# Kernel optimization log

Hardware: AMD Instinct MI355X
Metric: run time of the kernel (lower is better)

## Reference

```python
import jax, jax.numpy as jnp
import numpy as np

D = 2048
N_HEADS = 16
N_KV = 4
HEAD_DIM = D // N_HEADS  # 128
N_REP = N_HEADS // N_KV  # 4
B, S = 2, 2048


def setup_inputs() -> dict:
    key = jax.random.key(0)
    ks = jax.random.split(key, 5)
    scale = 0.02
    return {
        "x": jax.random.normal(ks[0], (B, S, D), dtype=jnp.float32),
        "wq": jax.random.normal(ks[1], (D, N_HEADS * HEAD_DIM), dtype=jnp.float32) * scale,
        "wk": jax.random.normal(ks[2], (D, N_KV * HEAD_DIM), dtype=jnp.float32) * scale,
        "wv": jax.random.normal(ks[3], (D, N_KV * HEAD_DIM), dtype=jnp.float32) * scale,
        "wo": jax.random.normal(ks[4], (N_HEADS * HEAD_DIM, D), dtype=jnp.float32) * scale,
    }


def reference(x, wq, wk, wv, wo):
    b, s, _ = x.shape
    # projections
    xq = (x @ wq).reshape(b, s, N_HEADS, HEAD_DIM)
    xk = (x @ wk).reshape(b, s, N_KV, HEAD_DIM)
    xv = (x @ wv).reshape(b, s, N_KV, HEAD_DIM)
    # GQA: group queries per kv head -> [b, n_kv, n_rep, s, d]
    xq = xq.transpose(0, 2, 1, 3).reshape(b, N_KV, N_REP, s, HEAD_DIM)
    xk = xk.transpose(0, 2, 1, 3)  # [b, n_kv, s, d]
    xv = xv.transpose(0, 2, 1, 3)
    scale = 1.0 / jnp.sqrt(jnp.asarray(HEAD_DIM, dtype=x.dtype))
    scores = jnp.einsum('bkrqd,bkvd->bkrqv', xq, xk) * scale  # [b,n_kv,n_rep,s,s]
    causal = jnp.triu(jnp.ones((s, s), dtype=bool), k=1)
    scores = jnp.where(causal, jnp.asarray(-jnp.inf, dtype=scores.dtype), scores)
    probs = jax.nn.softmax(scores, axis=-1)
    out = jnp.einsum('bkrqv,bkvd->bkrqd', probs, xv)  # [b,n_kv,n_rep,s,d]
    out = out.reshape(b, N_HEADS, s, HEAD_DIM).transpose(0, 2, 1, 3).reshape(b, s, N_HEADS * HEAD_DIM)
    return out @ wo
```

## Files before the change

### kernel.cpp

```cpp
#include <hip/hip_runtime.h>

typedef unsigned short u16;
using bf16x8 = __attribute__((ext_vector_type(8))) short;
using f32x4  = __attribute__((ext_vector_type(4))) float;

#define ATTN_NEG (-3.0e38f)

__device__ __forceinline__ u16 f2bf_rne(float f) {
  unsigned int u = __float_as_uint(f);
  u += 0x7fffu + ((u >> 16) & 1u);
  return (u16)(u >> 16);
}

__device__ __forceinline__ void load_lds16(const u16* g, u16* l) {
  using gp = const __attribute__((address_space(1))) unsigned int*;
  using lp = __attribute__((address_space(3))) unsigned int*;
  __builtin_amdgcn_global_load_lds((gp)g, (lp)l, 16, 0, 0);
}

__device__ __forceinline__ void transpose_body(const float* __restrict__ in,
                                               u16* __restrict__ out, int K, int N,
                                               int bx, int by, int tid) {
  __shared__ float tile[32][33];
  int tx = tid & 31, ty = tid >> 5;
  int x0 = bx * 32, y0 = by * 32;
  #pragma unroll
  for (int i = 0; i < 32; i += 8)
    tile[ty + i][tx] = in[(size_t)(y0 + ty + i) * N + x0 + tx];
  __syncthreads();
  #pragma unroll
  for (int i = 0; i < 32; i += 8)
    out[(size_t)(x0 + ty + i) * K + y0 + tx] = f2bf_rne(tile[tx][ty + i]);
}

__global__ __launch_bounds__(256) void prep_kernel(const float* __restrict__ x,
                                                   const float* __restrict__ wq,
                                                   const float* __restrict__ wk,
                                                   const float* __restrict__ wv,
                                                   const float* __restrict__ wo,
                                                   u16* xb, u16* wqt, u16* wkt, u16* wvt,
                                                   u16* wot) {
  int bid = blockIdx.x, tid = threadIdx.x;
  if (bid < 8192) {
    int i = bid * 1024 + tid * 4;
    float4 v = *(const float4*)(x + i);
    u16* p = xb + i;
    p[0] = f2bf_rne(v.x); p[1] = f2bf_rne(v.y); p[2] = f2bf_rne(v.z); p[3] = f2bf_rne(v.w);
  } else if (bid < 12288) {
    int t = bid - 8192;
    transpose_body(wq, wqt, 2048, 2048, t & 63, t >> 6, tid);
  } else if (bid < 13312) {
    int t = bid - 12288;
    transpose_body(wk, wkt, 2048, 512, t & 15, t >> 4, tid);
  } else if (bid < 14336) {
    int t = bid - 13312;
    transpose_body(wv, wvt, 2048, 512, t & 15, t >> 4, tid);
  } else {
    int t = bid - 14336;
    transpose_body(wo, wot, 2048, 2048, t & 63, t >> 6, tid);
  }
}

template <int MODE>
__device__ __forceinline__ void gemm_tile(const u16* __restrict__ A, const u16* __restrict__ Bt,
                                          void* __restrict__ Cv, int M, int N, int K,
                                          int bx, int by, char* smem) {
  u16* As = (u16*)smem;
  u16* Bs = (u16*)(smem + 16384);
  const int tid  = threadIdx.x;
  const int wave = tid >> 6, lane = tid & 63;
  const int quad = lane >> 4, l16 = lane & 15;
  const int m0 = by * 128, n0 = bx * 128;
  const int wm = (wave >> 1) * 64, wn = (wave & 1) * 64;
  f32x4 acc[4][4] = {};

  const int srow = lane >> 2;
  const int scol = (lane & 3) << 3;

  for (int k0 = 0; k0 < K; k0 += 64) {
    __syncthreads();
    #pragma unroll
    for (int h = 0; h < 2; ++h)
      #pragma unroll
      for (int i = 0; i < 2; ++i) {
        const int row = wave * 16 + i * 64;
        load_lds16(A  + (size_t)(m0 + row + srow) * K + k0 + h * 32 + scol,
                   As + h * 4096 + row * 32);
        load_lds16(Bt + (size_t)(n0 + row + srow) * K + k0 + h * 32 + scol,
                   Bs + h * 4096 + row * 32);
      }
    __syncthreads();
    #pragma unroll
    for (int h = 0; h < 2; ++h) {
      bf16x8 af[4], bfr[4];
      #pragma unroll
      for (int i = 0; i < 4; ++i) {
        af[i]  = *(const bf16x8*)(As + h * 4096 + (wm + i * 16 + l16) * 32 + quad * 8);
        bfr[i] = *(const bf16x8*)(Bs + h * 4096 + (wn + i * 16 + l16) * 32 + quad * 8);
      }
      #pragma unroll
      for (int mi = 0; mi < 4; ++mi)
        #pragma unroll
        for (int ni = 0; ni < 4; ++ni)
          acc[mi][ni] =
              __builtin_amdgcn_mfma_f32_16x16x32_bf16(af[mi], bfr[ni], acc[mi][ni], 0, 0, 0);
    }
  }

  if constexpr (MODE == 0 || MODE == 3) {
    const float sc = (MODE == 3) ? 0.12751742f : 1.0f;
    u16* Cb = (u16*)Cv;
    #pragma unroll
    for (int mi = 0; mi < 4; ++mi)
      #pragma unroll
      for (int ni = 0; ni < 4; ++ni) {
        int row = m0 + wm + mi * 16 + quad * 4;
        int col = n0 + wn + ni * 16 + l16;
        #pragma unroll
        for (int r = 0; r < 4; ++r)
          Cb[(size_t)(row + r) * N + col] = f2bf_rne(acc[mi][ni][r] * sc);
      }
  } else if constexpr (MODE == 1) {
    u16* Cb = (u16*)Cv;
    #pragma unroll
    for (int mi = 0; mi < 4; ++mi)
      #pragma unroll
      for (int ni = 0; ni < 4; ++ni) {
        int col = n0 + wn + ni * 16 + l16;
        #pragma unroll
        for (int r = 0; r < 4; ++r) {
          int row = m0 + wm + mi * 16 + quad * 4 + r;
          int bb = row >> 11, s = row & 2047;
          int c = s & 31;
          int cp = ((c & 15) >> 2) * 8 + ((c >> 4) & 1) * 4 + (c & 3);
          Cb[((size_t)(bb * 512 + col)) * 2048 + (s & ~31) + cp] = f2bf_rne(acc[mi][ni][r]);
        }
      }
  } else {
    float* Cf = (float*)Cv;
    #pragma unroll
    for (int mi = 0; mi < 4; ++mi)
      #pragma unroll
      for (int ni = 0; ni < 4; ++ni) {
        int row = m0 + wm + mi * 16 + quad * 4;
        int col = n0 + wn + ni * 16 + l16;
        #pragma unroll
        for (int r = 0; r < 4; ++r)
          Cf[(size_t)(row + r) * N + col] = acc[mi][ni][r];
      }
  }
}

__global__ __launch_bounds__(256) void qkv_gemm(const u16* xb, const u16* wqt, const u16* wkt,
                                                const u16* wvt, u16* Qb, u16* Kb, u16* Vt) {
  extern __shared__ char smem[];
  int bx = blockIdx.x, by = blockIdx.y;
  if (bx < 16)
    gemm_tile<3>(xb, wqt, Qb, 4096, 2048, 2048, bx, by, smem);
  else if (bx < 20)
    gemm_tile<0>(xb, wkt, Kb, 4096, 512, 2048, bx - 16, by, smem);
  else
    gemm_tile<1>(xb, wvt, Vt, 4096, 512, 2048, bx - 20, by, smem);
}

template <int MODE>
__global__ __launch_bounds__(256) void gemm_kernel(const u16* A, const u16* Bt, void* C,
                                                   int M, int N, int K) {
  extern __shared__ char smem[];
  gemm_tile<MODE>(A, Bt, C, M, N, K, blockIdx.x, blockIdx.y, smem);
}


__device__ __forceinline__ void stage_kv(const u16* __restrict__ Kg, const u16* __restrict__ Vg,
                                         int kt0, u16* __restrict__ kbuf, u16* __restrict__ vbuf,
                                         int wave, int quad, int l16) {
  #pragma unroll
  for (int h = 0; h < 2; ++h)
    load_lds16(Kg + (size_t)(kt0 + h * 16 + l16) * 512 + wave * 32 + quad * 8,
               kbuf + (wave * 2 + h) * 512);
  #pragma unroll
  for (int i = 0; i < 2; ++i) {
    int f = wave * 2 + i;
    load_lds16(Vg + (size_t)(16 * f + l16) * 2048 + kt0 + quad * 8, vbuf + f * 512);
  }
}

template <bool MASKED>
__device__ __forceinline__ void attn_compute2(const u16* __restrict__ kbuf,
                                              const u16* __restrict__ vbuf,
                                              int kt0, int q0w, int quad, int l16,
                                              const bf16x8 (&qfa)[4], const bf16x8 (&qfb)[4],
                                              f32x4 (&oa)[8], f32x4 (&ob)[8],
                                              float& la, float& lb) {
  const int slot = (quad * 16 + l16) * 8;
  bf16x8 kf[8];
  #pragma unroll
  for (int kk = 0; kk < 8; ++kk) kf[kk] = *(const bf16x8*)(kbuf + kk * 512 + slot);

  f32x4 sa[2] = {}, sb[2] = {};
  __builtin_amdgcn_s_setprio(1);
  #pragma unroll
  for (int h = 0; h < 2; ++h)
    #pragma unroll
    for (int ks = 0; ks < 4; ++ks) {
      sa[h] = __builtin_amdgcn_mfma_f32_16x16x32_bf16(kf[ks * 2 + h], qfa[ks], sa[h], 0, 0, 0);
      sb[h] = __builtin_amdgcn_mfma_f32_16x16x32_bf16(kf[ks * 2 + h], qfb[ks], sb[h], 0, 0, 0);
    }
  __builtin_amdgcn_s_setprio(0);

  bf16x8 pca, pcb;
  #pragma unroll
  for (int h = 0; h < 2; ++h)
    #pragma unroll
    for (int r = 0; r < 4; ++r) {
      int kpos = kt0 + 16 * h + quad * 4 + r;
      float s0 = sa[h][r], s1 = sb[h][r];
      if (MASKED) {
        s0 = (kpos <= q0w + l16) ? s0 : ATTN_NEG;
        s1 = (kpos <= q0w + 16 + l16) ? s1 : ATTN_NEG;
      }
      float p0 = __builtin_amdgcn_exp2f(s0);
      float p1 = __builtin_amdgcn_exp2f(s1);
      la += p0;
      lb += p1;
      pca[h * 4 + r] = (short)f2bf_rne(p0);
      pcb[h * 4 + r] = (short)f2bf_rne(p1);
    }

  __builtin_amdgcn_s_setprio(1);
  #pragma unroll
  for (int f = 0; f < 8; ++f) {
    bf16x8 v8 = *(const bf16x8*)(vbuf + f * 512 + slot);
    oa[f] = __builtin_amdgcn_mfma_f32_16x16x32_bf16(pca, v8, oa[f], 0, 0, 0);
    ob[f] = __builtin_amdgcn_mfma_f32_16x16x32_bf16(pcb, v8, ob[f], 0, 0, 0);
  }
  __builtin_amdgcn_s_setprio(0);
}

__global__ __launch_bounds__(256, 2) void attn_kernel(const u16* __restrict__ Qb,
                                                      const u16* __restrict__ Kb,
                                                      const u16* __restrict__ Vt,
                                                      u16* __restrict__ Ob) {
  constexpr int S = 2048;
  const int b = blockIdx.z, h = blockIdx.y, g = h >> 2;
  const int tile = b ? blockIdx.x : (15 - blockIdx.x);
  const int tid = threadIdx.x;
  const int wave = tid >> 6, lane = tid & 63, quad = lane >> 4, l16 = lane & 15;
  __shared__ alignas(16) u16 Kt[3][4096];
  __shared__ alignas(16) u16 Vl[3][4096];
  __shared__ float lbuf[4][2][16];

  const u16* Kg = Kb + (size_t)b * S * 512 + g * 128;
  const u16* Vg = Vt + (size_t)(b * 512 + g * 128) * 2048;

  const int q0w = tile * 128 + wave * 32;
  const int nsteps = 4 * tile + 4;
  const int s_diag = 4 * tile + wave;

  bf16x8 qfa[4], qfb[4];
  const u16* qra = Qb + (size_t)(b * S + q0w + l16) * 2048 + h * 128 + quad * 8;
  const u16* qrb = qra + (size_t)16 * 2048;
  #pragma unroll
  for (int ks = 0; ks < 4; ++ks) {
    qfa[ks] = *(const bf16x8*)(qra + ks * 32);
    qfb[ks] = *(const bf16x8*)(qrb + ks * 32);
  }
  asm volatile("s_waitcnt vmcnt(0)" ::: "memory");
  #pragma unroll
  for (int ks = 0; ks < 4; ++ks) {
    asm volatile("" : "+v"(qfa[ks]));
    asm volatile("" : "+v"(qfb[ks]));
  }

  f32x4 oa[8] = {}, ob[8] = {};
  float la = 0.f, lb = 0.f;

  stage_kv(Kg, Vg, 0, Kt[0], Vl[0], wave, quad, l16);
  stage_kv(Kg, Vg, 32, Kt[1], Vl[1], wave, quad, l16);

  for (int s = 0; s < nsteps; ++s) {
    asm volatile("s_waitcnt vmcnt(4)" ::: "memory");
    __builtin_amdgcn_s_barrier();
    {
      const int sn = (s + 2 < nsteps) ? s + 2 : nsteps - 1;
      const int bn = (s + 2) % 3;
      stage_kv(Kg, Vg, sn * 32, Kt[bn], Vl[bn], wave, quad, l16);
    }
    const int bc = s % 3;
    if (s < s_diag)
      attn_compute2<false>(Kt[bc], Vl[bc], s * 32, q0w, quad, l16, qfa, qfb, oa, ob, la, lb);
    else if (s == s_diag)
      attn_compute2<true>(Kt[bc], Vl[bc], s * 32, q0w, quad, l16, qfa, qfb, oa, ob, la, lb);
  }
  asm volatile("s_waitcnt vmcnt(0)" ::: "memory");

  float lta = la + __shfl_xor(la, 16);
  lta += __shfl_xor(lta, 32);
  float ltb = lb + __shfl_xor(lb, 16);
  ltb += __shfl_xor(ltb, 32);
  if (quad == 0) {
    lbuf[wave][0][l16] = lta;
    lbuf[wave][1][l16] = ltb;
  }
  __builtin_amdgcn_wave_barrier();
  float ila[4], ilb[4];
  #pragma unroll
  for (int r = 0; r < 4; ++r) {
    ila[r] = 1.f / lbuf[wave][0][quad * 4 + r];
    ilb[r] = 1.f / lbuf[wave][1][quad * 4 + r];
  }

  u16* ora = Ob + (size_t)(b * S + q0w + quad * 4) * 2048 + h * 128 + l16;
  u16* orb = ora + (size_t)16 * 2048;
  #pragma unroll
  for (int f = 0; f < 8; ++f)
    #pragma unroll
    for (int r = 0; r < 4; ++r) {
      ora[(size_t)r * 2048 + f * 16] = f2bf_rne(oa[f][r] * ila[r]);
      orb[(size_t)r * 2048 + f * 16] = f2bf_rne(ob[f][r] * ilb[r]);
    }
}

extern "C" void kernel_launch(void* const* d_in, const int* in_sizes, int n_in,
                              void* d_out, int out_size, void* d_ws, size_t ws_size,
                              hipStream_t stream) {
  const float* x  = (const float*)d_in[0];
  const float* wq = (const float*)d_in[1];
  const float* wk = (const float*)d_in[2];
  const float* wv = (const float*)d_in[3];
  const float* wo = (const float*)d_in[4];
  float* out = (float*)d_out;
  char* ws = (char*)d_ws;

  u16* xb  = (u16*)(ws);
  u16* wqt = (u16*)(ws + 16777216);
  u16* wkt = (u16*)(ws + 25165824);
  u16* wvt = (u16*)(ws + 27262976);
  u16* wot = (u16*)(ws + 29360128);
  u16* Qb  = (u16*)(ws + 37748736);
  u16* Kb  = (u16*)(ws + 54525952);
  u16* Vt  = (u16*)(ws + 58720256);
  u16* Ab  = (u16*)(ws + 62914560);

  prep_kernel<<<18432, 256, 0, stream>>>(x, wq, wk, wv, wo, xb, wqt, wkt, wvt, wot);
  qkv_gemm<<<dim3(24, 32), 256, 32768, stream>>>(xb, wqt, wkt, wvt, Qb, Kb, Vt);
  attn_kernel<<<dim3(16, 16, 2), 256, 0, stream>>>(Qb, Kb, Vt, Ab);
  gemm_kernel<2><<<dim3(16, 32), 256, 32768, stream>>>(Ab, wot, out, 4096, 2048, 2048);
}
```

Before: 311.6 us.

## Stage 64-key KV tiles with double buffering in attention loop

Each pipeline step now stages and consumes 64 keys instead of 32. The three-buffer ring and explicit vmcnt waits are replaced by a two-buffer ping-pong guarded by __syncthreads. Inside a 64-key step the diagonal mask is applied per 32-key half, and masked halves are skipped with an early break. The goal is to halve the number of barriers and loop iterations. In exchange it relies on __syncthreads to drain the async LDS loads, which may serialize more than the previous finer vmcnt(4) waits, and it doubles LDS per buffer.

```diff
diff --git a/kernel.cpp b/kernel.cpp
--- a/kernel.cpp
+++ b/kernel.cpp
@@ -171,70 +171,82 @@
 }
 
 
-__device__ __forceinline__ void stage_kv(const u16* __restrict__ Kg, const u16* __restrict__ Vg,
-                                         int kt0, u16* __restrict__ kbuf, u16* __restrict__ vbuf,
-                                         int wave, int quad, int l16) {
-  #pragma unroll
-  for (int h = 0; h < 2; ++h)
-    load_lds16(Kg + (size_t)(kt0 + h * 16 + l16) * 512 + wave * 32 + quad * 8,
-               kbuf + (wave * 2 + h) * 512);
-  #pragma unroll
-  for (int i = 0; i < 2; ++i) {
-    int f = wave * 2 + i;
-    load_lds16(Vg + (size_t)(16 * f + l16) * 2048 + kt0 + quad * 8, vbuf + f * 512);
+__device__ __forceinline__ void stage_kv64(const u16* __restrict__ Kg, const u16* __restrict__ Vg,
+                                           int kt0, u16* __restrict__ kbuf,
+                                           u16* __restrict__ vbuf,
+                                           int wave, int quad, int l16) {
+  #pragma unroll
+  for (int c = 0; c < 2; ++c) {
+    #pragma unroll
+    for (int h = 0; h < 2; ++h)
+      load_lds16(Kg + (size_t)(kt0 + 32 * c + h * 16 + l16) * 512 + wave * 32 + quad * 8,
+                 kbuf + c * 4096 + (wave * 2 + h) * 512);
+    #pragma unroll
+    for (int i = 0; i < 2; ++i) {
+      int f = wave * 2 + i;
+      load_lds16(Vg + (size_t)(16 * f + l16) * 2048 + kt0 + 32 * c + quad * 8,
+                 vbuf + c * 4096 + f * 512);
+    }
   }
 }
 
 template <bool MASKED>
-__device__ __forceinline__ void attn_compute2(const u16* __restrict__ kbuf,
-                                              const u16* __restrict__ vbuf,
-                                              int kt0, int q0w, int quad, int l16,
-                                              const bf16x8 (&qfa)[4], const bf16x8 (&qfb)[4],
-                                              f32x4 (&oa)[8], f32x4 (&ob)[8],
-                                              float& la, float& lb) {
+__device__ __forceinline__ void attn_compute64q2(const u16* __restrict__ kbuf,
+                                                 const u16* __restrict__ vbuf,
+                                                 int kt0, int q0w, int quad, int l16,
+                                                 const bf16x8 (&qfa)[4], const bf16x8 (&qfb)[4],
+                                                 f32x4 (&oa)[8], f32x4 (&ob)[8],
+                                                 float& la, float& lb) {
   const int slot = (quad * 16 + l16) * 8;
-  bf16x8 kf[8];
-  #pragma unroll
-  for (int kk = 0; kk < 8; ++kk) kf[kk] = *(const bf16x8*)(kbuf + kk * 512 + slot);
-
-  f32x4 sa[2] = {}, sb[2] = {};
-  __builtin_amdgcn_s_setprio(1);
-  #pragma unroll
-  for (int h = 0; h < 2; ++h)
-    #pragma unroll
-    for (int ks = 0; ks < 4; ++ks) {
-      sa[h] = __builtin_amdgcn_mfma_f32_16x16x32_bf16(kf[ks * 2 + h], qfa[ks], sa[h], 0, 0, 0);
-      sb[h] = __builtin_amdgcn_mfma_f32_16x16x32_bf16(kf[ks * 2 + h], qfb[ks], sb[h], 0, 0, 0);
+  #pragma unroll
+  for (int c = 0; c < 2; ++c) {
+    const int kb = kt0 + 32 * c;
+    if (MASKED && kb > q0w + 31) break;
+
+    bf16x8 kf[8];
+    #pragma unroll
+    for (int kk = 0; kk < 8; ++kk)
+      kf[kk] = *(const bf16x8*)(kbuf + c * 4096 + kk * 512 + slot);
+
+    f32x4 sa[2] = {}, sb[2] = {};
+    __builtin_amdgcn_s_setprio(1);
+    #pragma unroll
+    for (int h = 0; h < 2; ++h)
+      #pragma unroll
+      for (int ks = 0; ks < 4; ++ks) {
+        sa[h] = __builtin_amdgcn_mfma_f32_16x16x32_bf16(kf[ks * 2 + h], qfa[ks], sa[h], 0, 0, 0);
+        sb[h] = __builtin_amdgcn_mfma_f32_16x16x32_bf16(kf[ks * 2 + h], qfb[ks], sb[h], 0, 0, 0);
+      }
+    __builtin_amdgcn_s_setprio(0);
+
+    bf16x8 pca, pcb;
+    #pragma unroll
+    for (int h = 0; h < 2; ++h)
+      #pragma unroll
+      for (int r = 0; r < 4; ++r) {
+        int kpos = kb + 16 * h + quad * 4 + r;
+        float s0 = sa[h][r], s1 = sb[h][r];
+        if (MASKED) {
+          s0 = (kpos <= q0w + l16) ? s0 : ATTN_NEG;
+          s1 = (kpos <= q0w + 16 + l16) ? s1 : ATTN_NEG;
+        }
+        float p0 = __builtin_amdgcn_exp2f(s0);
+        float p1 = __builtin_amdgcn_exp2f(s1);
+        la += p0;
+        lb += p1;
+        pca[h * 4 + r] = (short)f2bf_rne(p0);
+        pcb[h * 4 + r] = (short)f2bf_rne(p1);
+      }
+
+    __builtin_amdgcn_s_setprio(1);
+    #pragma unroll
+    for (int f = 0; f < 8; ++f) {
+      bf16x8 v8 = *(const bf16x8*)(vbuf + c * 4096 + f * 512 + slot);
+      oa[f] = __builtin_amdgcn_mfma_f32_16x16x32_bf16(pca, v8, oa[f], 0, 0, 0);
+      ob[f] = __builtin_amdgcn_mfma_f32_16x16x32_bf16(pcb, v8, ob[f], 0, 0, 0);
     }
-  __builtin_amdgcn_s_setprio(0);
-
-  bf16x8 pca, pcb;
-  #pragma unroll
-  for (int h = 0; h < 2; ++h)
-    #pragma unroll
-    for (int r = 0; r < 4; ++r) {
-      int kpos = kt0 + 16 * h + quad * 4 + r;
-      float s0 = sa[h][r], s1 = sb[h][r];
-      if (MASKED) {
-        s0 = (kpos <= q0w + l16) ? s0 : ATTN_NEG;
-        s1 = (kpos <= q0w + 16 + l16) ? s1 : ATTN_NEG;
-      }
-      float p0 = __builtin_amdgcn_exp2f(s0);
-      float p1 = __builtin_amdgcn_exp2f(s1);
-      la += p0;
-      lb += p1;
-      pca[h * 4 + r] = (short)f2bf_rne(p0);
-      pcb[h * 4 + r] = (short)f2bf_rne(p1);
-    }
-
-  __builtin_amdgcn_s_setprio(1);
-  #pragma unroll
-  for (int f = 0; f < 8; ++f) {
-    bf16x8 v8 = *(const bf16x8*)(vbuf + f * 512 + slot);
-    oa[f] = __builtin_amdgcn_mfma_f32_16x16x32_bf16(pca, v8, oa[f], 0, 0, 0);
-    ob[f] = __builtin_amdgcn_mfma_f32_16x16x32_bf16(pcb, v8, ob[f], 0, 0, 0);
-  }
-  __builtin_amdgcn_s_setprio(0);
+    __builtin_amdgcn_s_setprio(0);
+  }
 }
 
 __global__ __launch_bounds__(256, 2) void attn_kernel(const u16* __restrict__ Qb,
@@ -246,16 +258,15 @@
   const int tile = b ? blockIdx.x : (15 - blockIdx.x);
   const int tid = threadIdx.x;
   const int wave = tid >> 6, lane = tid & 63, quad = lane >> 4, l16 = lane & 15;
-  __shared__ alignas(16) u16 Kt[3][4096];
-  __shared__ alignas(16) u16 Vl[3][4096];
+  __shared__ alignas(16) u16 Kt[2][8192];
+  __shared__ alignas(16) u16 Vl[2][8192];
   __shared__ float lbuf[4][2][16];
 
   const u16* Kg = Kb + (size_t)b * S * 512 + g * 128;
   const u16* Vg = Vt + (size_t)(b * 512 + g * 128) * 2048;
 
   const int q0w = tile * 128 + wave * 32;
-  const int nsteps = 4 * tile + 4;
-  const int s_diag = 4 * tile + wave;
+  const int nsteps = 2 * tile + 2;
 
   bf16x8 qfa[4], qfb[4];
   const u16* qra = Qb + (size_t)(b * S + q0w + l16) * 2048 + h * 128 + quad * 8;
@@ -265,34 +276,23 @@
     qfa[ks] = *(const bf16x8*)(qra + ks * 32);
     qfb[ks] = *(const bf16x8*)(qrb + ks * 32);
   }
-  asm volatile("s_waitcnt vmcnt(0)" ::: "memory");
-  #pragma unroll
-  for (int ks = 0; ks < 4; ++ks) {
-    asm volatile("" : "+v"(qfa[ks]));
-    asm volatile("" : "+v"(qfb[ks]));
-  }
 
   f32x4 oa[8] = {}, ob[8] = {};
   float la = 0.f, lb = 0.f;
 
-  stage_kv(Kg, Vg, 0, Kt[0], Vl[0], wave, quad, l16);
-  stage_kv(Kg, Vg, 32, Kt[1], Vl[1], wave, quad, l16);
+  stage_kv64(Kg, Vg, 0, Kt[0], Vl[0], wave, quad, l16);
 
   for (int s = 0; s < nsteps; ++s) {
-    asm volatile("s_waitcnt vmcnt(4)" ::: "memory");
-    __builtin_amdgcn_s_barrier();
-    {
-      const int sn = (s + 2 < nsteps) ? s + 2 : nsteps - 1;
-      const int bn = (s + 2) % 3;
-      stage_kv(Kg, Vg, sn * 32, Kt[bn], Vl[bn], wave, quad, l16);
-    }
-    const int bc = s % 3;
-    if (s < s_diag)
-      attn_compute2<false>(Kt[bc], Vl[bc], s * 32, q0w, quad, l16, qfa, qfb, oa, ob, la, lb);
-    else if (s == s_diag)
-      attn_compute2<true>(Kt[bc], Vl[bc], s * 32, q0w, quad, l16, qfa, qfb, oa, ob, la, lb);
-  }
-  asm volatile("s_waitcnt vmcnt(0)" ::: "memory");
+    __syncthreads();
+    if (s + 1 < nsteps)
+      stage_kv64(Kg, Vg, (s + 1) * 64, Kt[(s + 1) & 1], Vl[(s + 1) & 1], wave, quad, l16);
+    if (64 * s + 63 <= q0w)
+      attn_compute64q2<false>(Kt[s & 1], Vl[s & 1], s * 64, q0w, quad, l16, qfa, qfb,
+                              oa, ob, la, lb);
+    else if (64 * s <= q0w + 31)
+      attn_compute64q2<true>(Kt[s & 1], Vl[s & 1], s * 64, q0w, quad, l16, qfa, qfb,
+                             oa, ob, la, lb);
+  }
 
   float lta = la + __shfl_xor(la, 16);
   lta += __shfl_xor(lta, 32);
```

Result: faster. 300.7 us (-3.5%).
